# Kernel tuning notes

Hardware: AMD Instinct MI355X
Metric: run time of the kernel (lower is better)

Reference implementation:

```python
import jax, jax.numpy as jnp
import numpy as np

CR = 32  # channels // reduction

def setup_inputs() -> dict:
    key = jax.random.key(0)
    k1, k2 = jax.random.split(key)
    x = jax.random.normal(k1, (1, 64, 8, 32, 32), dtype=jnp.float32)
    W = jax.random.normal(k2, (CR, 64), dtype=jnp.float32) * (1.0 / np.sqrt(64.0))
    bias = jnp.zeros((CR,), dtype=jnp.float32)
    return {"x": x, "W": W, "bias": bias}

def reference(x, W, bias):
    b, c, d, h, w = x.shape
    cr = W.shape[0]
    n = d * h * w
    # 1x1x1 Conv3d == per-voxel linear projection over channels
    x_red = jnp.einsum('oc,bcdhw->bodhw', W, x) + bias[None, :, None, None, None]
    q = x_red.reshape(b, cr, n)          # [b, cr, N]
    k = q                                 # shared projection (q == k)
    v = x.reshape(b, c, n)               # [b, c, N]
    # attn[b, i, j] = <q[:, i], k[:, j]>, softmax over j (dim=2)
    attn = jnp.einsum('bci,bcj->bij', q, k) / jnp.sqrt(jnp.float32(cr))
    attn = jax.nn.softmax(attn, axis=2)
    # out[b, c, m] = sum_n v[b, c, n] * attn[b, n, m]  (torch.bmm(v, attn))
    out = jnp.einsum('bcn,bnm->bcm', v, attn)
    out = out.reshape(b, c, d, h, w)
    return out + x
```

## Files before the change

### kernel.cpp

```cpp
#include <hip/hip_runtime.h>

#define N_TOK 8192

typedef _Float16 f16x8 __attribute__((ext_vector_type(8)));
typedef _Float16 f16x4 __attribute__((ext_vector_type(4)));
typedef float    f32x4 __attribute__((ext_vector_type(4)));

__device__ __forceinline__ f32x4 mfma16(f16x8 a, f16x8 b, f32x4 c) {
  return __builtin_amdgcn_mfma_f32_16x16x32_f16(a, b, c, 0, 0, 0);
}

#define QSCALE 0.50500977f

__global__ __launch_bounds__(256) void prep_kernel(
    const float* __restrict__ x, const float* __restrict__ W,
    const float* __restrict__ bias, _Float16* __restrict__ qe,
    _Float16* __restrict__ vh) {
  int blk = blockIdx.x, t = threadIdx.x;
  if (blk < 1024) {
    __shared__ float Wl[32 * 65];
    for (int i = t; i < 2048; i += 256) Wl[(i >> 6) * 65 + (i & 63)] = W[i];
    __syncthreads();
    int g = blk * 256 + t;
    int o = g & 31, n = g >> 5;
    float acc0 = bias[o], acc1 = 0.f;
#pragma unroll
    for (int c = 0; c < 32; ++c) {
      acc0 = fmaf(Wl[o * 65 + c], x[c * N_TOK + n], acc0);
      acc1 = fmaf(Wl[o * 65 + 32 + c], x[(32 + c) * N_TOK + n], acc1);
    }
    qe[n * 32 + o] = (_Float16)((acc0 + acc1) * QSCALE);
  } else {
    int i4 = (blk - 1024) * 256 + t;
    f32x4 v = ((const f32x4*)x)[i4];
    f16x4 h;
#pragma unroll
    for (int j = 0; j < 4; ++j) h[j] = (_Float16)v[j];
    *(f16x4*)(vh + i4 * 4) = h;
  }
}

__global__ __launch_bounds__(512) void pass1_kernel(
    const _Float16* __restrict__ qe, float* __restrict__ Bn) {
  __shared__ float Lp[8][32];
  int t = threadIdx.x;
  int w = t >> 6, lane = t & 63, quad = lane >> 4, l15 = lane & 15;
  int n0 = blockIdx.x * 32;
  f16x8 af0 = *(const f16x8*)(qe + (n0 + l15) * 32 + quad * 8);
  f16x8 af1 = *(const f16x8*)(qe + (n0 + 16 + l15) * 32 + quad * 8);
  f32x4 sums0 = {0.f, 0.f, 0.f, 0.f}, sums1 = {0.f, 0.f, 0.f, 0.f};
  for (int mt = 0; mt < 64; ++mt) {
    int m0 = w * 1024 + mt * 16;
    f16x8 bf = *(const f16x8*)(qe + (m0 + l15) * 32 + quad * 8);
    f32x4 zero = {0.f, 0.f, 0.f, 0.f};
    f32x4 s0 = mfma16(af0, bf, zero);
    f32x4 s1 = mfma16(af1, bf, zero);
#pragma unroll
    for (int r = 0; r < 4; ++r) {
      sums0[r] += __builtin_amdgcn_exp2f(s0[r]);
      sums1[r] += __builtin_amdgcn_exp2f(s1[r]);
    }
  }
#pragma unroll
  for (int r = 0; r < 4; ++r) {
#pragma unroll
    for (int mask = 1; mask < 16; mask <<= 1) {
      sums0[r] += __shfl_xor(sums0[r], mask, 64);
      sums1[r] += __shfl_xor(sums1[r], mask, 64);
    }
  }
  if (l15 == 0) {
    *(f32x4*)&Lp[w][quad * 4] = sums0;
    *(f32x4*)&Lp[w][16 + quad * 4] = sums1;
  }
  __syncthreads();
  if (t < 32) {
    float L = 0.f;
#pragma unroll
    for (int ww = 0; ww < 8; ++ww) L += Lp[ww][t];
    Bn[n0 + t] = __builtin_amdgcn_logf(L);
  }
}

__global__ __launch_bounds__(1024) void pass2_kernel(
    const _Float16* __restrict__ qe, const _Float16* __restrict__ vh,
    const float* __restrict__ Bn, const float* __restrict__ x,
    float* __restrict__ out) {
  __shared__ _Float16 Pt[16 * 1280];
  __shared__ float Ot[8 * 64 * 33];
  int t = threadIdx.x;
  int w = t >> 6, lane = t & 63, quad = lane >> 4, l15 = lane & 15;
  int m0 = blockIdx.x * 32;
  _Float16* myP = Pt + w * 1280;

  f16x8 bm0 = *(const f16x8*)(qe + (m0 + l15) * 32 + quad * 8);
  f16x8 bm1 = *(const f16x8*)(qe + (m0 + 16 + l15) * 32 + quad * 8);

  f32x4 acc[4][2];
#pragma unroll
  for (int ct = 0; ct < 4; ++ct)
#pragma unroll
    for (int mt = 0; mt < 2; ++mt) acc[ct][mt] = f32x4{0.f, 0.f, 0.f, 0.f};

  for (int ch = 0; ch < 16; ++ch) {
    int nb = w * 512 + ch * 32;
    f16x8 an[2];
    an[0] = *(const f16x8*)(qe + (nb + l15) * 32 + quad * 8);
    an[1] = *(const f16x8*)(qe + (nb + 16 + l15) * 32 + quad * 8);
    f32x4 Bq[2];
    Bq[0] = *(const f32x4*)(Bn + nb + quad * 4);
    Bq[1] = *(const f32x4*)(Bn + nb + 16 + quad * 4);
    __asm__ volatile("s_waitcnt lgkmcnt(0)" ::: "memory");
#pragma unroll
    for (int nt = 0; nt < 2; ++nt) {
      f16x8 a = an[nt];
#pragma unroll
      for (int mt = 0; mt < 2; ++mt) {
        f32x4 zero = {0.f, 0.f, 0.f, 0.f};
        f32x4 s = mfma16(a, (mt == 0) ? bm0 : bm1, zero);
        f16x4 p;
#pragma unroll
        for (int r = 0; r < 4; ++r)
          p[r] = (_Float16)__builtin_amdgcn_exp2f(s[r] - Bq[nt][r]);
        *(f16x4*)(myP + (mt * 16 + l15) * 40 + nt * 16 + quad * 4) = p;
      }
    }
    __asm__ volatile("s_waitcnt lgkmcnt(0)" ::: "memory");
    f16x8 bp0 = *(const f16x8*)(myP + l15 * 40 + quad * 8);
    f16x8 bp1 = *(const f16x8*)(myP + (16 + l15) * 40 + quad * 8);
#pragma unroll
    for (int ct = 0; ct < 4; ++ct) {
      f16x8 av = *(const f16x8*)(vh + (ct * 16 + l15) * N_TOK + nb + quad * 8);
      acc[ct][0] = mfma16(av, bp0, acc[ct][0]);
      acc[ct][1] = mfma16(av, bp1, acc[ct][1]);
    }
  }

  if (w < 8) {
#pragma unroll
    for (int ct = 0; ct < 4; ++ct)
#pragma unroll
      for (int mt = 0; mt < 2; ++mt)
#pragma unroll
        for (int r = 0; r < 4; ++r)
          Ot[(w * 64 + ct * 16 + quad * 4 + r) * 33 + mt * 16 + l15] =
              acc[ct][mt][r];
  }
  __syncthreads();
  if (w >= 8) {
#pragma unroll
    for (int ct = 0; ct < 4; ++ct)
#pragma unroll
      for (int mt = 0; mt < 2; ++mt)
#pragma unroll
        for (int r = 0; r < 4; ++r)
          Ot[((w - 8) * 64 + ct * 16 + quad * 4 + r) * 33 + mt * 16 + l15] +=
              acc[ct][mt][r];
  }
  __syncthreads();
  for (int idx = t; idx < 2048; idx += 1024) {
    int cc = idx >> 5, m = idx & 31;
    float v = 0.f;
#pragma unroll
    for (int s = 0; s < 8; ++s) v += Ot[(s * 64 + cc) * 33 + m];
    out[cc * N_TOK + m0 + m] = v + x[cc * N_TOK + m0 + m];
  }
}

extern "C" void kernel_launch(void* const* d_in, const int* in_sizes, int n_in,
                              void* d_out, int out_size, void* d_ws,
                              size_t ws_size, hipStream_t stream) {
  const float* x = (const float*)d_in[0];
  const float* W = (const float*)d_in[1];
  const float* bias = (const float*)d_in[2];
  float* out = (float*)d_out;

  char* ws = (char*)d_ws;
  _Float16* qe = (_Float16*)ws;
  _Float16* vh = (_Float16*)(ws + 524288);
  float* Bn = (float*)(ws + 524288 + 1048576);

  prep_kernel<<<1536, 256, 0, stream>>>(x, W, bias, qe, vh);
  pass1_kernel<<<256, 512, 0, stream>>>(qe, Bn);
  pass2_kernel<<<256, 1024, 0, stream>>>(qe, vh, Bn, x, out);
}
```

Before: 113.9 us.

## Tile prep projection in LDS, register-prefetch pass1, and keep P in registers in pass2

The prep kernel now stages a 64-token x tile in shared memory and has each thread compute 8 tokens for one output channel, so x is reused across channels. Pass1 processes two key tiles per iteration with a software-prefetched next load. Pass2 drops the shared-memory P staging: probabilities stay in registers and feed 16x16x16 MFMAs directly, next-chunk q/Bn loads are double-buffered, and the block shrinks from 16 to 8 waves with a 4-block occupancy hint. These changes aim to cut LDS traffic, barrier waits and global load latency, at the cost of higher register pressure and less parallelism per block.

```diff
diff --git a/kernel.cpp b/kernel.cpp
--- a/kernel.cpp
+++ b/kernel.cpp
@@ -6,8 +6,11 @@
 typedef _Float16 f16x4 __attribute__((ext_vector_type(4)));
 typedef float    f32x4 __attribute__((ext_vector_type(4)));
 
-__device__ __forceinline__ f32x4 mfma16(f16x8 a, f16x8 b, f32x4 c) {
+__device__ __forceinline__ f32x4 mfma_k32(f16x8 a, f16x8 b, f32x4 c) {
   return __builtin_amdgcn_mfma_f32_16x16x32_f16(a, b, c, 0, 0, 0);
+}
+__device__ __forceinline__ f32x4 mfma_k16(f16x4 a, f16x4 b, f32x4 c) {
+  return __builtin_amdgcn_mfma_f32_16x16x16f16(a, b, c, 0, 0, 0);
 }
 
 #define QSCALE 0.50500977f
@@ -17,21 +20,33 @@
     const float* __restrict__ bias, _Float16* __restrict__ qe,
     _Float16* __restrict__ vh) {
   int blk = blockIdx.x, t = threadIdx.x;
-  if (blk < 1024) {
+  if (blk < 128) {
     __shared__ float Wl[32 * 65];
+    __shared__ float xs[64 * 72];
     for (int i = t; i < 2048; i += 256) Wl[(i >> 6) * 65 + (i & 63)] = W[i];
+    int n0 = blk * 64;
+#pragma unroll
+    for (int rr = 0; rr < 16; ++rr) {
+      int c = rr * 4 + (t >> 6);
+      xs[c * 72 + (t & 63)] = x[c * N_TOK + n0 + (t & 63)];
+    }
     __syncthreads();
-    int g = blk * 256 + t;
-    int o = g & 31, n = g >> 5;
-    float acc0 = bias[o], acc1 = 0.f;
-#pragma unroll
-    for (int c = 0; c < 32; ++c) {
-      acc0 = fmaf(Wl[o * 65 + c], x[c * N_TOK + n], acc0);
-      acc1 = fmaf(Wl[o * 65 + 32 + c], x[(32 + c) * N_TOK + n], acc1);
-    }
-    qe[n * 32 + o] = (_Float16)((acc0 + acc1) * QSCALE);
+    int o = t & 31, ns = t >> 5;
+    float acc[8];
+    float bv = bias[o];
+#pragma unroll
+    for (int i = 0; i < 8; ++i) acc[i] = bv;
+    for (int c = 0; c < 64; ++c) {
+      float wv = Wl[o * 65 + c];
+#pragma unroll
+      for (int i = 0; i < 8; ++i)
+        acc[i] = fmaf(wv, xs[c * 72 + ns + i * 8], acc[i]);
+    }
+#pragma unroll
+    for (int i = 0; i < 8; ++i)
+      qe[(n0 + ns + i * 8) * 32 + o] = (_Float16)(acc[i] * QSCALE);
   } else {
-    int i4 = (blk - 1024) * 256 + t;
+    int i4 = (blk - 128) * 256 + t;
     f32x4 v = ((const f32x4*)x)[i4];
     f16x4 h;
 #pragma unroll
@@ -48,19 +63,30 @@
   int n0 = blockIdx.x * 32;
   f16x8 af0 = *(const f16x8*)(qe + (n0 + l15) * 32 + quad * 8);
   f16x8 af1 = *(const f16x8*)(qe + (n0 + 16 + l15) * 32 + quad * 8);
-  f32x4 sums0 = {0.f, 0.f, 0.f, 0.f}, sums1 = {0.f, 0.f, 0.f, 0.f};
-  for (int mt = 0; mt < 64; ++mt) {
-    int m0 = w * 1024 + mt * 16;
-    f16x8 bf = *(const f16x8*)(qe + (m0 + l15) * 32 + quad * 8);
-    f32x4 zero = {0.f, 0.f, 0.f, 0.f};
-    f32x4 s0 = mfma16(af0, bf, zero);
-    f32x4 s1 = mfma16(af1, bf, zero);
+  const _Float16* qb = qe + (w * 1024 + l15) * 32 + quad * 8;
+  f16x8 pb0 = *(const f16x8*)(qb);
+  f16x8 pb1 = *(const f16x8*)(qb + 512);
+  f32x4 a00 = {0.f, 0.f, 0.f, 0.f}, a01 = a00, a10 = a00, a11 = a00;
+  for (int mt = 0; mt < 32; ++mt) {
+    f16x8 b0 = pb0, b1 = pb1;
+    int nx = ((mt + 1) & 31) * 1024;
+    pb0 = *(const f16x8*)(qb + nx);
+    pb1 = *(const f16x8*)(qb + nx + 512);
+    f32x4 z = {0.f, 0.f, 0.f, 0.f};
+    f32x4 s00 = mfma_k32(af0, b0, z);
+    f32x4 s01 = mfma_k32(af0, b1, z);
+    f32x4 s10 = mfma_k32(af1, b0, z);
+    f32x4 s11 = mfma_k32(af1, b1, z);
 #pragma unroll
     for (int r = 0; r < 4; ++r) {
-      sums0[r] += __builtin_amdgcn_exp2f(s0[r]);
-      sums1[r] += __builtin_amdgcn_exp2f(s1[r]);
-    }
-  }
+      a00[r] += __builtin_amdgcn_exp2f(s00[r]);
+      a01[r] += __builtin_amdgcn_exp2f(s01[r]);
+      a10[r] += __builtin_amdgcn_exp2f(s10[r]);
+      a11[r] += __builtin_amdgcn_exp2f(s11[r]);
+    }
+  }
+  f32x4 sums0 = a00 + a01;
+  f32x4 sums1 = a10 + a11;
 #pragma unroll
   for (int r = 0; r < 4; ++r) {
 #pragma unroll
@@ -82,61 +108,76 @@
   }
 }
 
-__global__ __launch_bounds__(1024) void pass2_kernel(
+__global__ __launch_bounds__(512, 4) void pass2_kernel(
     const _Float16* __restrict__ qe, const _Float16* __restrict__ vh,
     const float* __restrict__ Bn, const float* __restrict__ x,
     float* __restrict__ out) {
-  __shared__ _Float16 Pt[16 * 1280];
-  __shared__ float Ot[8 * 64 * 33];
+  __shared__ float Ot[4 * 64 * 33];
   int t = threadIdx.x;
   int w = t >> 6, lane = t & 63, quad = lane >> 4, l15 = lane & 15;
   int m0 = blockIdx.x * 32;
-  _Float16* myP = Pt + w * 1280;
 
   f16x8 bm0 = *(const f16x8*)(qe + (m0 + l15) * 32 + quad * 8);
   f16x8 bm1 = *(const f16x8*)(qe + (m0 + 16 + l15) * 32 + quad * 8);
 
+  int base = w * 1024;
+  const _Float16* qa = qe + (base + l15) * 32 + quad * 8;
+  const float* bnb = Bn + base + quad * 4;
+  const _Float16* vb = vh + l15 * N_TOK + base + quad * 4;
+
   f32x4 acc[4][2];
 #pragma unroll
   for (int ct = 0; ct < 4; ++ct)
 #pragma unroll
     for (int mt = 0; mt < 2; ++mt) acc[ct][mt] = f32x4{0.f, 0.f, 0.f, 0.f};
 
-  for (int ch = 0; ch < 16; ++ch) {
-    int nb = w * 512 + ch * 32;
-    f16x8 an[2];
-    an[0] = *(const f16x8*)(qe + (nb + l15) * 32 + quad * 8);
-    an[1] = *(const f16x8*)(qe + (nb + 16 + l15) * 32 + quad * 8);
-    f32x4 Bq[2];
-    Bq[0] = *(const f32x4*)(Bn + nb + quad * 4);
-    Bq[1] = *(const f32x4*)(Bn + nb + 16 + quad * 4);
-    __asm__ volatile("s_waitcnt lgkmcnt(0)" ::: "memory");
-#pragma unroll
-    for (int nt = 0; nt < 2; ++nt) {
-      f16x8 a = an[nt];
-#pragma unroll
-      for (int mt = 0; mt < 2; ++mt) {
-        f32x4 zero = {0.f, 0.f, 0.f, 0.f};
-        f32x4 s = mfma16(a, (mt == 0) ? bm0 : bm1, zero);
-        f16x4 p;
-#pragma unroll
-        for (int r = 0; r < 4; ++r)
-          p[r] = (_Float16)__builtin_amdgcn_exp2f(s[r] - Bq[nt][r]);
-        *(f16x4*)(myP + (mt * 16 + l15) * 40 + nt * 16 + quad * 4) = p;
-      }
-    }
-    __asm__ volatile("s_waitcnt lgkmcnt(0)" ::: "memory");
-    f16x8 bp0 = *(const f16x8*)(myP + l15 * 40 + quad * 8);
-    f16x8 bp1 = *(const f16x8*)(myP + (16 + l15) * 40 + quad * 8);
+  f16x8 anb[2][2];
+  f32x4 Bqb[2][2];
+  anb[0][0] = *(const f16x8*)(qa);
+  anb[0][1] = *(const f16x8*)(qa + 512);
+  Bqb[0][0] = *(const f32x4*)(bnb);
+  Bqb[0][1] = *(const f32x4*)(bnb + 16);
+
+#pragma unroll 2
+  for (int ch = 0; ch < 32; ++ch) {
+    int cur = ch & 1, nxt = cur ^ 1;
+    int rnx = ((ch + 1) & 31) * 32;
+    anb[nxt][0] = *(const f16x8*)(qa + rnx * 32);
+    anb[nxt][1] = *(const f16x8*)(qa + rnx * 32 + 512);
+    Bqb[nxt][0] = *(const f32x4*)(bnb + rnx);
+    Bqb[nxt][1] = *(const f32x4*)(bnb + rnx + 16);
+
+    int rc = ch * 32;
+    f16x4 av[4][2];
+#pragma unroll
+    for (int ct = 0; ct < 4; ++ct)
+#pragma unroll
+      for (int nt = 0; nt < 2; ++nt)
+        av[ct][nt] = *(const f16x4*)(vb + ct * 16 * N_TOK + rc + nt * 16);
+
+    f32x4 z = {0.f, 0.f, 0.f, 0.f};
+    f32x4 s00 = mfma_k32(anb[cur][0], bm0, z);
+    f32x4 s01 = mfma_k32(anb[cur][0], bm1, z);
+    f32x4 s10 = mfma_k32(anb[cur][1], bm0, z);
+    f32x4 s11 = mfma_k32(anb[cur][1], bm1, z);
+    f16x4 p00, p01, p10, p11;
+#pragma unroll
+    for (int r = 0; r < 4; ++r) {
+      p00[r] = (_Float16)__builtin_amdgcn_exp2f(s00[r] - Bqb[cur][0][r]);
+      p01[r] = (_Float16)__builtin_amdgcn_exp2f(s01[r] - Bqb[cur][0][r]);
+      p10[r] = (_Float16)__builtin_amdgcn_exp2f(s10[r] - Bqb[cur][1][r]);
+      p11[r] = (_Float16)__builtin_amdgcn_exp2f(s11[r] - Bqb[cur][1][r]);
+    }
 #pragma unroll
     for (int ct = 0; ct < 4; ++ct) {
-      f16x8 av = *(const f16x8*)(vh + (ct * 16 + l15) * N_TOK + nb + quad * 8);
-      acc[ct][0] = mfma16(av, bp0, acc[ct][0]);
-      acc[ct][1] = mfma16(av, bp1, acc[ct][1]);
-    }
-  }
-
-  if (w < 8) {
+      acc[ct][0] = mfma_k16(av[ct][0], p00, acc[ct][0]);
+      acc[ct][1] = mfma_k16(av[ct][0], p01, acc[ct][1]);
+      acc[ct][0] = mfma_k16(av[ct][1], p10, acc[ct][0]);
+      acc[ct][1] = mfma_k16(av[ct][1], p11, acc[ct][1]);
+    }
+  }
+
+  if (w < 4) {
 #pragma unroll
     for (int ct = 0; ct < 4; ++ct)
 #pragma unroll
@@ -147,22 +188,22 @@
               acc[ct][mt][r];
   }
   __syncthreads();
-  if (w >= 8) {
+  if (w >= 4) {
 #pragma unroll
     for (int ct = 0; ct < 4; ++ct)
 #pragma unroll
       for (int mt = 0; mt < 2; ++mt)
 #pragma unroll
         for (int r = 0; r < 4; ++r)
-          Ot[((w - 8) * 64 + ct * 16 + quad * 4 + r) * 33 + mt * 16 + l15] +=
+          Ot[((w - 4) * 64 + ct * 16 + quad * 4 + r) * 33 + mt * 16 + l15] +=
               acc[ct][mt][r];
   }
   __syncthreads();
-  for (int idx = t; idx < 2048; idx += 1024) {
+  for (int idx = t; idx < 2048; idx += 512) {
     int cc = idx >> 5, m = idx & 31;
     float v = 0.f;
 #pragma unroll
-    for (int s = 0; s < 8; ++s) v += Ot[(s * 64 + cc) * 33 + m];
+    for (int s = 0; s < 4; ++s) v += Ot[(s * 64 + cc) * 33 + m];
     out[cc * N_TOK + m0 + m] = v + x[cc * N_TOK + m0 + m];
   }
 }
@@ -180,7 +221,7 @@
   _Float16* vh = (_Float16*)(ws + 524288);
   float* Bn = (float*)(ws + 524288 + 1048576);
 
-  prep_kernel<<<1536, 256, 0, stream>>>(x, W, bias, qe, vh);
+  prep_kernel<<<640, 256, 0, stream>>>(x, W, bias, qe, vh);
   pass1_kernel<<<256, 512, 0, stream>>>(qe, Bn);
-  pass2_kernel<<<256, 1024, 0, stream>>>(qe, vh, Bn, x, out);
-}
+  pass2_kernel<<<256, 512, 0, stream>>>(qe, vh, Bn, x, out);
+}
```

Result: slower. 142.8 us (+25.4%).
